# Kernel optimization log

Measured on AMD Instinct MI355X. Metric: run time of the kernel, lower is better.

The kernel has to match this reference:

```python
import jax, jax.numpy as jnp
import numpy as np

B, N, D, H, K = 8, 256, 128, 128, 8


def _kaiming_uniform(key, shape, fan_in):
    bound = np.sqrt(6.0 / fan_in)
    return jax.random.uniform(key, shape, jnp.float32, -bound, bound)


def setup_inputs() -> dict:
    key = jax.random.key(0)
    ks = jax.random.split(key, 5)
    E = jax.random.normal(ks[0], (B, N, D), jnp.float32)
    W1 = _kaiming_uniform(ks[1], (K, 2 * D, H), 2 * D)   # FFN2 layer 1
    b1 = jnp.zeros((K, H), jnp.float32)
    W2 = _kaiming_uniform(ks[2], (K, H, 2), H)           # FFN2 layer 2
    b2 = jnp.zeros((K, 2), jnp.float32)
    W3 = _kaiming_uniform(ks[3], (K, 2, 1), 2)           # FFN3
    b3 = jnp.zeros((K, 1), jnp.float32)
    return {"E": E, "W1": W1, "b1": b1, "W2": W2, "b2": b2, "W3": W3, "b3": b3}


def _entmax15_pair(logits):
    # Exact alpha=1.5 entmax over a last dim of size 2 (closed form).
    # z' = z/2; p_i = [z'_i - tau]_+^2 with sum(p)=1.
    t = (logits[..., 0] - logits[..., 1]) * 0.25   # signed half-gap of z'
    d = jnp.abs(t)
    s = jnp.sqrt(jnp.maximum(0.5 - d * d, 0.0))
    p0_interior = (s + t) ** 2                      # both coords in support
    p0 = jnp.where(d >= 0.5, (t > 0).astype(logits.dtype), p0_interior)
    return jnp.stack([p0, 1.0 - p0], axis=-1)


def reference(E, W1, b1, W2, b2, W3, b3):
    # E: [B,N,D]. Concat([Ei,Ej]) @ W1 == Ei @ W1[:D] + Ej @ W1[D:], so we never
    # materialize the [B,N,N,2D] pair tensor.
    Dd = E.shape[-1]
    W1i, W1j = W1[:, :Dd, :], W1[:, Dd:, :]
    outs = []
    for h in range(W1.shape[0]):  # small fixed head loop (k_basis)
        hi = jnp.einsum('bnd,dh->bnh', E, W1i[h])
        hj = jnp.einsum('bnd,dh->bnh', E, W1j[h])
        pre = hi[:, :, None, :] + hj[:, None, :, :] + b1[h]      # [B,N,N,H]
        act = jax.nn.relu(pre)                                    # dropout: eval mode (identity)
        logits2 = jnp.einsum('bijh,hc->bijc', act, W2[h]) + b2[h]  # [B,N,N,2]
        p2 = _entmax15_pair(logits2)
        a = jnp.einsum('bijc,co->bijo', p2, W3[h])[..., 0] + b3[h][0]  # [B,N,N]
        outs.append(a)
    M = jnp.stack(outs, axis=1)  # [B,K,N,N]
    n = E.shape[1]
    eye = jnp.eye(n, dtype=M.dtype)
    M = M * (1.0 - eye)[None, None]  # no_self_loop=True
    return M
```

## Files before the change

### kernel.cpp

```cpp
#include <hip/hip_runtime.h>
#include <hip/hip_fp16.h>
#include <cstdint>
#include <cstddef>

#define B_ 8
#define N_ 256
#define D_ 128
#define H_ 128
#define K_ 8

typedef _Float16 f16x8 __attribute__((ext_vector_type(8)));
typedef _Float16 f16x2 __attribute__((ext_vector_type(2)));
typedef float    f32x4 __attribute__((ext_vector_type(4)));

static __device__ __forceinline__ f16x2 h2cast(unsigned u) {
    return __builtin_bit_cast(f16x2, u);
}
static __device__ __forceinline__ unsigned packh2(float lo, float hi) {
    unsigned a = __half_as_ushort(__float2half(lo));
    unsigned b = __half_as_ushort(__float2half(hi));
    return a | (b << 16);
}

__global__ __launch_bounds__(256) void prep_all(
        const float* __restrict__ E, const float* __restrict__ W1,
        const float* __restrict__ W2, const float* __restrict__ b2,
        const float* __restrict__ W3, const float* __restrict__ b3,
        __half* __restrict__ Eh, __half* __restrict__ Wh,
        unsigned* __restrict__ wdh, float* __restrict__ consts) {
    __shared__ float Ws[128][33];
    const int bid = blockIdx.x;
    const int t   = threadIdx.x;

    if (bid < 256) {
        int idx = (bid * 256 + t) * 4;
        float4 v = *(const float4*)&E[idx];
        uint2 o;
        o.x = packh2(v.x, v.y);
        o.y = packh2(v.z, v.w);
        *(uint2*)&Eh[idx] = o;
    } else if (bid < 320) {
        const int kb = bid - 256;
        const int ct = kb & 7;
        const int k  = kb >> 3;
        const int c0 = ct * 32;
        const int ro = (c0 < 128) ? 0 : 128;
        const int h0 = c0 & 127;
        #pragma unroll
        for (int rep = 0; rep < 16; rep++) {
            int idx = rep * 256 + t;
            int d   = idx >> 5;
            int cl  = idx & 31;
            Ws[d][cl] = W1[((size_t)(k * 256 + ro + d)) * H_ + h0 + cl];
        }
        __syncthreads();
        const int cl = t >> 3;
        const int dg = t & 7;
        __half tmp[16];
        #pragma unroll
        for (int e = 0; e < 16; e++) tmp[e] = __float2half(Ws[dg * 16 + e][cl]);
        *(float4*)&Wh[((size_t)(k * 256 + c0 + cl)) * D_ + dg * 16]     = *(float4*)&tmp[0];
        *(float4*)&Wh[((size_t)(k * 256 + c0 + cl)) * D_ + dg * 16 + 8] = *(float4*)&tmp[8];
    } else {
        for (int idx = t; idx < K_ * 64; idx += 256) {
            int base = idx * 2;
            float w0 = W2[base * 2]     - W2[base * 2 + 1];
            float w1 = W2[base * 2 + 2] - W2[base * 2 + 3];
            wdh[idx] = packh2(w0, w1);
        }
        if (t < K_) {
            consts[t * 4 + 0] = b2[t * 2] - b2[t * 2 + 1];
            consts[t * 4 + 1] = W3[t * 2] - W3[t * 2 + 1];
            consts[t * 4 + 2] = W3[t * 2 + 1] + b3[t];
        }
    }
}

__global__ __launch_bounds__(256, 2) void fused_kernel(
        const __half* __restrict__ Eh, const __half* __restrict__ Wh,
        const float* __restrict__ b1, const unsigned* __restrict__ wdh,
        const float* __restrict__ consts, float* __restrict__ out) {
    __shared__ __half his[128 * 136];
    __shared__ __half hjs[64 * 136];
    __shared__ unsigned wlds[64];

    const int bid = blockIdx.x;
    const int jt  = bid & 3;
    const int it  = (bid >> 2) & 1;
    const int bk  = bid >> 3;
    const int k   = bk & (K_ - 1);
    const int b   = bk >> 3;
    const int i0  = it * 128, j0 = jt * 64;
    const int t   = threadIdx.x;
    const int wv   = t >> 6;
    const int lane = t & 63;
    const int lr   = lane & 15, lk = lane >> 4;

    if (t < 64) wlds[t] = wdh[k * 64 + t];

    #pragma unroll
    for (int rb = 0; rb < 3; rb++) {
        const int row16 = wv * 48 + rb * 16;
        const bool isJ  = (row16 >= 128);
        const int rowg  = isJ ? (j0 + row16 - 128) : (i0 + row16);
        const int cbase = isJ ? 128 : 0;
        __half* __restrict__ dst = isJ ? &hjs[(row16 - 128) * 136] : &his[row16 * 136];

        f16x8 A[4];
        #pragma unroll
        for (int kk = 0; kk < 4; kk++)
            A[kk] = *(const f16x8*)&Eh[
                ((size_t)(b * N_ + rowg + lr)) * D_ + kk * 32 + lk * 8];

        #pragma unroll
        for (int nc = 0; nc < 8; nc++) {
            f16x8 Bf[4];
            #pragma unroll
            for (int kk = 0; kk < 4; kk++)
                Bf[kk] = *(const f16x8*)&Wh[
                    ((size_t)(k * 256 + cbase + nc * 16 + lr)) * D_ + kk * 32 + lk * 8];
            const int hcol = nc * 16 + lr;
            const float bias = isJ ? 0.f : b1[k * H_ + hcol];
            f32x4 acc = {0.f, 0.f, 0.f, 0.f};
            #pragma unroll
            for (int kk = 0; kk < 4; kk++)
                acc = __builtin_amdgcn_mfma_f32_16x16x32_f16(A[kk], Bf[kk], acc, 0, 0, 0);
            #pragma unroll
            for (int q = 0; q < 4; q++)
                dst[(lk * 4 + q) * 136 + hcol] = __float2half(acc[q] + bias);
        }
    }
    __syncthreads();

    const float b2d = consts[k * 4 + 0];
    const float w3d = consts[k * 4 + 1];
    const float w3b = consts[k * 4 + 2];
    const int tx = t & 15;
    const int ty = t >> 4;

    float acc[8][4];
    #pragma unroll
    for (int a = 0; a < 8; a++)
        #pragma unroll
        for (int c = 0; c < 4; c++) acc[a][c] = b2d;

    const f16x2 zz = {(_Float16)0, (_Float16)0};

    #pragma unroll 2
    for (int hq = 0; hq < 16; hq++) {
        unsigned Wv[4];
        *(uint4*)&Wv[0] = *(const uint4*)&wlds[hq * 4];
        unsigned Aa[8][4], Bb[4][4];
        #pragma unroll
        for (int a = 0; a < 8; a++)
            *(uint4*)&Aa[a][0] = *(const uint4*)&his[(ty + 16 * a) * 136 + hq * 8];
        #pragma unroll
        for (int c = 0; c < 4; c++)
            *(uint4*)&Bb[c][0] = *(const uint4*)&hjs[(tx + 16 * c) * 136 + hq * 8];

        #pragma unroll
        for (int e = 0; e < 4; e++) {
            f16x2 w2 = h2cast(Wv[e]);
            #pragma unroll
            for (int a = 0; a < 8; a++) {
                f16x2 av = h2cast(Aa[a][e]);
                #pragma unroll
                for (int c = 0; c < 4; c++) {
                    f16x2 pre = av + h2cast(Bb[c][e]);
                    f16x2 act = __builtin_elementwise_max(pre, zz);
                    acc[a][c] = __builtin_amdgcn_fdot2(act, w2, acc[a][c], false);
                }
            }
        }
    }

    #pragma unroll
    for (int a = 0; a < 8; a++) {
        int i = i0 + ty + 16 * a;
        #pragma unroll
        for (int c = 0; c < 4; c++) {
            float av = acc[a][c];
            float tt = av * 0.25f;
            float dd = fabsf(tt);
            float ss = sqrtf(fmaxf(0.5f - dd * dd, 0.f));
            float p0i = (ss + tt) * (ss + tt);
            float p0 = (dd >= 0.5f) ? (tt > 0.f ? 1.f : 0.f) : p0i;
            float val = fmaf(p0, w3d, w3b);
            int j = j0 + tx + 16 * c;
            if (i == j) val = 0.f;
            out[((size_t)bk * N_ + i) * N_ + j] = val;
        }
    }
}

extern "C" void kernel_launch(void* const* d_in, const int* in_sizes, int n_in,
                              void* d_out, int out_size, void* d_ws, size_t ws_size,
                              hipStream_t stream) {
    (void)in_sizes; (void)n_in; (void)out_size; (void)ws_size;
    const float* E  = (const float*)d_in[0];
    const float* W1 = (const float*)d_in[1];
    const float* b1 = (const float*)d_in[2];
    const float* W2 = (const float*)d_in[3];
    const float* b2 = (const float*)d_in[4];
    const float* W3 = (const float*)d_in[5];
    const float* b3 = (const float*)d_in[6];
    float* out = (float*)d_out;

    char* ws = (char*)d_ws;
    unsigned* wdh    = (unsigned*)ws;
    float*    consts = (float*)(ws + 4096);
    __half*   Eh     = (__half*)(ws + 8192);
    __half*   Wh     = (__half*)(ws + 8192 + 524288);

    prep_all<<<321, 256, 0, stream>>>(E, W1, W2, b2, W3, b3, Eh, Wh, wdh, consts);
    fused_kernel<<<B_ * K_ * 8, 256, 0, stream>>>(Eh, Wh, b1, wdh, consts, out);
}
```

Baseline: 58.78 us.

## Rewrite ReLU-weighted sum as abs-sum plus separable linear terms

Uses relu(x)=(x+|x|)/2 to split the pairwise hidden reduction into a per-row term, a per-column term, and a sign-weighted sum of absolute values. The |w2| scale is folded into the projected i/j features, so the inner loop does one add and one abs-FMA per hidden unit. The j-side features are now kept in fp32 shared memory and the accumulation is done in scalar fp32 rather than packed fp16 dot2. This removes the max and weight multiply per pair but gives up the 2-wide packed fp16 throughput and increases LDS use.

```diff
diff --git a/kernel.cpp b/kernel.cpp
--- a/kernel.cpp
+++ b/kernel.cpp
@@ -10,12 +10,8 @@
 #define K_ 8
 
 typedef _Float16 f16x8 __attribute__((ext_vector_type(8)));
-typedef _Float16 f16x2 __attribute__((ext_vector_type(2)));
 typedef float    f32x4 __attribute__((ext_vector_type(4)));
 
-static __device__ __forceinline__ f16x2 h2cast(unsigned u) {
-    return __builtin_bit_cast(f16x2, u);
-}
 static __device__ __forceinline__ unsigned packh2(float lo, float hi) {
     unsigned a = __half_as_ushort(__float2half(lo));
     unsigned b = __half_as_ushort(__float2half(hi));
@@ -27,7 +23,8 @@
         const float* __restrict__ W2, const float* __restrict__ b2,
         const float* __restrict__ W3, const float* __restrict__ b3,
         __half* __restrict__ Eh, __half* __restrict__ Wh,
-        unsigned* __restrict__ wdh, float* __restrict__ consts) {
+        float* __restrict__ mW, float* __restrict__ wdaW,
+        float* __restrict__ consts) {
     __shared__ float Ws[128][33];
     const int bid = blockIdx.x;
     const int t   = threadIdx.x;
@@ -62,11 +59,10 @@
         *(float4*)&Wh[((size_t)(k * 256 + c0 + cl)) * D_ + dg * 16]     = *(float4*)&tmp[0];
         *(float4*)&Wh[((size_t)(k * 256 + c0 + cl)) * D_ + dg * 16 + 8] = *(float4*)&tmp[8];
     } else {
-        for (int idx = t; idx < K_ * 64; idx += 256) {
-            int base = idx * 2;
-            float w0 = W2[base * 2]     - W2[base * 2 + 1];
-            float w1 = W2[base * 2 + 2] - W2[base * 2 + 3];
-            wdh[idx] = packh2(w0, w1);
+        for (int idx = t; idx < K_ * H_; idx += 256) {
+            float w = W2[idx * 2] - W2[idx * 2 + 1];
+            mW[idx]   = copysignf(1.0f, w);
+            wdaW[idx] = 0.5f * fabsf(w);
         }
         if (t < K_) {
             consts[t * 4 + 0] = b2[t * 2] - b2[t * 2 + 1];
@@ -78,11 +74,15 @@
 
 __global__ __launch_bounds__(256, 2) void fused_kernel(
         const __half* __restrict__ Eh, const __half* __restrict__ Wh,
-        const float* __restrict__ b1, const unsigned* __restrict__ wdh,
-        const float* __restrict__ consts, float* __restrict__ out) {
+        const float* __restrict__ b1, const float* __restrict__ mW,
+        const float* __restrict__ wdaW, const float* __restrict__ consts,
+        float* __restrict__ out) {
     __shared__ __half his[128 * 136];
-    __shared__ __half hjs[64 * 136];
-    __shared__ unsigned wlds[64];
+    __shared__ float  hjs[64 * 132];
+    __shared__ float  mlds[128];
+    __shared__ float  wlds[128];
+    __shared__ float  ulds[128];
+    __shared__ float  vlds[64];
 
     const int bid = blockIdx.x;
     const int jt  = bid & 3;
@@ -96,7 +96,8 @@
     const int lane = t & 63;
     const int lr   = lane & 15, lk = lane >> 4;
 
-    if (t < 64) wlds[t] = wdh[k * 64 + t];
+    if (t < 128) { mlds[t] = mW[k * H_ + t]; wlds[t] = wdaW[k * H_ + t]; }
+    __syncthreads();
 
     #pragma unroll
     for (int rb = 0; rb < 3; rb++) {
@@ -104,7 +105,6 @@
         const bool isJ  = (row16 >= 128);
         const int rowg  = isJ ? (j0 + row16 - 128) : (i0 + row16);
         const int cbase = isJ ? 128 : 0;
-        __half* __restrict__ dst = isJ ? &hjs[(row16 - 128) * 136] : &his[row16 * 136];
 
         f16x8 A[4];
         #pragma unroll
@@ -120,15 +120,48 @@
                 Bf[kk] = *(const f16x8*)&Wh[
                     ((size_t)(k * 256 + cbase + nc * 16 + lr)) * D_ + kk * 32 + lk * 8];
             const int hcol = nc * 16 + lr;
-            const float bias = isJ ? 0.f : b1[k * H_ + hcol];
             f32x4 acc = {0.f, 0.f, 0.f, 0.f};
             #pragma unroll
             for (int kk = 0; kk < 4; kk++)
                 acc = __builtin_amdgcn_mfma_f32_16x16x32_f16(A[kk], Bf[kk], acc, 0, 0, 0);
-            #pragma unroll
-            for (int q = 0; q < 4; q++)
-                dst[(lk * 4 + q) * 136 + hcol] = __float2half(acc[q] + bias);
-        }
+            const float sc = wlds[hcol];
+            if (isJ) {
+                #pragma unroll
+                for (int q = 0; q < 4; q++)
+                    hjs[(row16 - 128 + lk * 4 + q) * 132 + hcol] = acc[q] * sc;
+            } else {
+                const float bias = b1[k * H_ + hcol];
+                #pragma unroll
+                for (int q = 0; q < 4; q++)
+                    his[(row16 + lk * 4 + q) * 136 + hcol] =
+                        __float2half((acc[q] + bias) * sc);
+            }
+        }
+    }
+    __syncthreads();
+
+    if (t < 128) {
+        float s = 0.f;
+        #pragma unroll
+        for (int hq = 0; hq < 16; hq++) {
+            f16x8 av = *(const f16x8*)&his[t * 136 + hq * 8];
+            #pragma unroll
+            for (int e = 0; e < 8; e++) s += (float)av[e] * mlds[hq * 8 + e];
+        }
+        ulds[t] = s;
+    } else if (t < 192) {
+        const int r = t - 128;
+        float s = 0.f;
+        #pragma unroll
+        for (int hq = 0; hq < 16; hq++) {
+            float4 b0 = *(const float4*)&hjs[r * 132 + hq * 8];
+            float4 b1v = *(const float4*)&hjs[r * 132 + hq * 8 + 4];
+            s += b0.x * mlds[hq * 8 + 0] + b0.y * mlds[hq * 8 + 1]
+               + b0.z * mlds[hq * 8 + 2] + b0.w * mlds[hq * 8 + 3]
+               + b1v.x * mlds[hq * 8 + 4] + b1v.y * mlds[hq * 8 + 5]
+               + b1v.z * mlds[hq * 8 + 6] + b1v.w * mlds[hq * 8 + 7];
+        }
+        vlds[r] = s;
     }
     __syncthreads();
 
@@ -142,51 +175,55 @@
     #pragma unroll
     for (int a = 0; a < 8; a++)
         #pragma unroll
-        for (int c = 0; c < 4; c++) acc[a][c] = b2d;
-
-    const f16x2 zz = {(_Float16)0, (_Float16)0};
+        for (int c = 0; c < 4; c++) acc[a][c] = 0.f;
 
     #pragma unroll 2
     for (int hq = 0; hq < 16; hq++) {
-        unsigned Wv[4];
-        *(uint4*)&Wv[0] = *(const uint4*)&wlds[hq * 4];
-        unsigned Aa[8][4], Bb[4][4];
+        float mv[8];
+        *(float4*)&mv[0] = *(const float4*)&mlds[hq * 8];
+        *(float4*)&mv[4] = *(const float4*)&mlds[hq * 8 + 4];
+        f16x8 Ah[8];
         #pragma unroll
         for (int a = 0; a < 8; a++)
-            *(uint4*)&Aa[a][0] = *(const uint4*)&his[(ty + 16 * a) * 136 + hq * 8];
-        #pragma unroll
-        for (int c = 0; c < 4; c++)
-            *(uint4*)&Bb[c][0] = *(const uint4*)&hjs[(tx + 16 * c) * 136 + hq * 8];
-
-        #pragma unroll
-        for (int e = 0; e < 4; e++) {
-            f16x2 w2 = h2cast(Wv[e]);
-            #pragma unroll
-            for (int a = 0; a < 8; a++) {
-                f16x2 av = h2cast(Aa[a][e]);
+            Ah[a] = *(const f16x8*)&his[(ty + 16 * a) * 136 + hq * 8];
+        float Bf[4][8];
+        #pragma unroll
+        for (int c = 0; c < 4; c++) {
+            *(float4*)&Bf[c][0] = *(const float4*)&hjs[(tx + 16 * c) * 132 + hq * 8];
+            *(float4*)&Bf[c][4] = *(const float4*)&hjs[(tx + 16 * c) * 132 + hq * 8 + 4];
+        }
+        #pragma unroll
+        for (int e = 0; e < 8; e++) {
+            float Ae[8];
+            #pragma unroll
+            for (int a = 0; a < 8; a++) Ae[a] = (float)Ah[a][e];
+            #pragma unroll
+            for (int a = 0; a < 8; a++)
                 #pragma unroll
-                for (int c = 0; c < 4; c++) {
-                    f16x2 pre = av + h2cast(Bb[c][e]);
-                    f16x2 act = __builtin_elementwise_max(pre, zz);
-                    acc[a][c] = __builtin_amdgcn_fdot2(act, w2, acc[a][c], false);
-                }
-            }
-        }
-    }
+                for (int c = 0; c < 4; c++)
+                    acc[a][c] = fmaf(mv[e], fabsf(Ae[a] + Bf[c][e]), acc[a][c]);
+        }
+    }
+
+    float ua[8], vc[4];
+    #pragma unroll
+    for (int a = 0; a < 8; a++) ua[a] = ulds[ty + 16 * a];
+    #pragma unroll
+    for (int c = 0; c < 4; c++) vc[c] = vlds[tx + 16 * c];
 
     #pragma unroll
     for (int a = 0; a < 8; a++) {
-        int i = i0 + ty + 16 * a;
+        const int i = i0 + ty + 16 * a;
         #pragma unroll
         for (int c = 0; c < 4; c++) {
-            float av = acc[a][c];
-            float tt = av * 0.25f;
+            float T = b2d + ua[a] + vc[c] + acc[a][c];
+            float tt = T * 0.25f;
             float dd = fabsf(tt);
             float ss = sqrtf(fmaxf(0.5f - dd * dd, 0.f));
             float p0i = (ss + tt) * (ss + tt);
             float p0 = (dd >= 0.5f) ? (tt > 0.f ? 1.f : 0.f) : p0i;
             float val = fmaf(p0, w3d, w3b);
-            int j = j0 + tx + 16 * c;
+            const int j = j0 + tx + 16 * c;
             if (i == j) val = 0.f;
             out[((size_t)bk * N_ + i) * N_ + j] = val;
         }
@@ -207,11 +244,12 @@
     float* out = (float*)d_out;
 
     char* ws = (char*)d_ws;
-    unsigned* wdh    = (unsigned*)ws;
-    float*    consts = (float*)(ws + 4096);
-    __half*   Eh     = (__half*)(ws + 8192);
-    __half*   Wh     = (__half*)(ws + 8192 + 524288);
-
-    prep_all<<<321, 256, 0, stream>>>(E, W1, W2, b2, W3, b3, Eh, Wh, wdh, consts);
-    fused_kernel<<<B_ * K_ * 8, 256, 0, stream>>>(Eh, Wh, b1, wdh, consts, out);
-}
+    float*  mW     = (float*)ws;
+    float*  wdaW   = (float*)(ws + 4096);
+    float*  consts = (float*)(ws + 8192);
+    __half* Eh     = (__half*)(ws + 12288);
+    __half* Wh     = (__half*)(ws + 12288 + 524288);
+
+    prep_all<<<321, 256, 0, stream>>>(E, W1, W2, b2, W3, b3, Eh, Wh, mW, wdaW, consts);
+    fused_kernel<<<B_ * K_ * 8, 256, 0, stream>>>(Eh, Wh, b1, mW, wdaW, consts, out);
+}
```

Measured after the change: 73.30 us. 24.7% more time.

## Shrink output tile to 64x64 with 512 threads for more blocks and occupancy

Applied to the files above, without the earlier changes.

Changes the fused kernel from 128x64 output tiles with 256 threads to 64x64 tiles with 512 threads. The grid doubles to 1024 blocks, and each thread now holds 2x4 accumulators instead of 8x4. Each wave computes one 16-row projection strip in a single pass instead of looping over three. The goal is more parallelism, lower register pressure and higher occupancy (launch bounds 512,8). The cost is that the hi/hj projection work is recomputed across more tiles, and each thread reuses its shared-memory loads less.

```diff
diff --git a/kernel.cpp b/kernel.cpp
--- a/kernel.cpp
+++ b/kernel.cpp
@@ -76,21 +76,21 @@
     }
 }
 
-__global__ __launch_bounds__(256, 2) void fused_kernel(
+__global__ __launch_bounds__(512, 8) void fused_kernel(
         const __half* __restrict__ Eh, const __half* __restrict__ Wh,
         const float* __restrict__ b1, const unsigned* __restrict__ wdh,
         const float* __restrict__ consts, float* __restrict__ out) {
-    __shared__ __half his[128 * 136];
-    __shared__ __half hjs[64 * 136];
-    __shared__ unsigned wlds[64];
+    __shared__ __attribute__((aligned(16))) __half his[64 * 136];
+    __shared__ __attribute__((aligned(16))) __half hjs[64 * 136];
+    __shared__ __attribute__((aligned(16))) unsigned wlds[64];
 
     const int bid = blockIdx.x;
     const int jt  = bid & 3;
-    const int it  = (bid >> 2) & 1;
-    const int bk  = bid >> 3;
+    const int it  = (bid >> 2) & 3;
+    const int bk  = bid >> 4;
     const int k   = bk & (K_ - 1);
     const int b   = bk >> 3;
-    const int i0  = it * 128, j0 = jt * 64;
+    const int i0  = it * 64, j0 = jt * 64;
     const int t   = threadIdx.x;
     const int wv   = t >> 6;
     const int lane = t & 63;
@@ -98,19 +98,17 @@
 
     if (t < 64) wlds[t] = wdh[k * 64 + t];
 
-    #pragma unroll
-    for (int rb = 0; rb < 3; rb++) {
-        const int row16 = wv * 48 + rb * 16;
-        const bool isJ  = (row16 >= 128);
-        const int rowg  = isJ ? (j0 + row16 - 128) : (i0 + row16);
-        const int cbase = isJ ? 128 : 0;
-        __half* __restrict__ dst = isJ ? &hjs[(row16 - 128) * 136] : &his[row16 * 136];
+    {
+        const bool isJ  = (wv >= 4);
+        const int  grp  = isJ ? (wv - 4) : wv;
+        const int  rowg = (isJ ? j0 : i0) + grp * 16 + lr;
+        const int  cbase = isJ ? 128 : 0;
+        __half* __restrict__ dst = isJ ? hjs : his;
 
         f16x8 A[4];
         #pragma unroll
         for (int kk = 0; kk < 4; kk++)
-            A[kk] = *(const f16x8*)&Eh[
-                ((size_t)(b * N_ + rowg + lr)) * D_ + kk * 32 + lk * 8];
+            A[kk] = *(const f16x8*)&Eh[((size_t)(b * N_ + rowg)) * D_ + kk * 32 + lk * 8];
 
         #pragma unroll
         for (int nc = 0; nc < 8; nc++) {
@@ -127,7 +125,7 @@
                 acc = __builtin_amdgcn_mfma_f32_16x16x32_f16(A[kk], Bf[kk], acc, 0, 0, 0);
             #pragma unroll
             for (int q = 0; q < 4; q++)
-                dst[(lk * 4 + q) * 136 + hcol] = __float2half(acc[q] + bias);
+                dst[(grp * 16 + lk * 4 + q) * 136 + hcol] = __float2half(acc[q] + bias);
         }
     }
     __syncthreads();
@@ -135,12 +133,12 @@
     const float b2d = consts[k * 4 + 0];
     const float w3d = consts[k * 4 + 1];
     const float w3b = consts[k * 4 + 2];
-    const int tx = t & 15;
-    const int ty = t >> 4;
-
-    float acc[8][4];
+    const int tx  = t & 15;
+    const int tyy = t >> 4;
+
+    float acc[2][4];
     #pragma unroll
-    for (int a = 0; a < 8; a++)
+    for (int a = 0; a < 2; a++)
         #pragma unroll
         for (int c = 0; c < 4; c++) acc[a][c] = b2d;
 
@@ -150,10 +148,10 @@
     for (int hq = 0; hq < 16; hq++) {
         unsigned Wv[4];
         *(uint4*)&Wv[0] = *(const uint4*)&wlds[hq * 4];
-        unsigned Aa[8][4], Bb[4][4];
-        #pragma unroll
-        for (int a = 0; a < 8; a++)
-            *(uint4*)&Aa[a][0] = *(const uint4*)&his[(ty + 16 * a) * 136 + hq * 8];
+        unsigned Aa[2][4], Bb[4][4];
+        #pragma unroll
+        for (int a = 0; a < 2; a++)
+            *(uint4*)&Aa[a][0] = *(const uint4*)&his[(tyy + 32 * a) * 136 + hq * 8];
         #pragma unroll
         for (int c = 0; c < 4; c++)
             *(uint4*)&Bb[c][0] = *(const uint4*)&hjs[(tx + 16 * c) * 136 + hq * 8];
@@ -162,7 +160,7 @@
         for (int e = 0; e < 4; e++) {
             f16x2 w2 = h2cast(Wv[e]);
             #pragma unroll
-            for (int a = 0; a < 8; a++) {
+            for (int a = 0; a < 2; a++) {
                 f16x2 av = h2cast(Aa[a][e]);
                 #pragma unroll
                 for (int c = 0; c < 4; c++) {
@@ -175,8 +173,8 @@
     }
 
     #pragma unroll
-    for (int a = 0; a < 8; a++) {
-        int i = i0 + ty + 16 * a;
+    for (int a = 0; a < 2; a++) {
+        const int i = i0 + tyy + 32 * a;
         #pragma unroll
         for (int c = 0; c < 4; c++) {
             float av = acc[a][c];
@@ -186,7 +184,7 @@
             float p0i = (ss + tt) * (ss + tt);
             float p0 = (dd >= 0.5f) ? (tt > 0.f ? 1.f : 0.f) : p0i;
             float val = fmaf(p0, w3d, w3b);
-            int j = j0 + tx + 16 * c;
+            const int j = j0 + tx + 16 * c;
             if (i == j) val = 0.f;
             out[((size_t)bk * N_ + i) * N_ + j] = val;
         }
@@ -213,5 +211,5 @@
     __half*   Wh     = (__half*)(ws + 8192 + 524288);
 
     prep_all<<<321, 256, 0, stream>>>(E, W1, W2, b2, W3, b3, Eh, Wh, wdh, consts);
-    fused_kernel<<<B_ * K_ * 8, 256, 0, stream>>>(Eh, Wh, b1, wdh, consts, out);
-}
+    fused_kernel<<<B_ * K_ * 16, 512, 0, stream>>>(Eh, Wh, b1, wdh, consts, out);
+}
```

After: 57.31 us. 2.5% less time.
